# Kernel optimization log

Measured on AMD Instinct MI355X. Metric: run time of the kernel, lower is better.

The kernel has to match this reference:

```python
import jax, jax.numpy as jnp
import numpy as np

N = 100_000      # nodes
E = 3_200_000    # edges (avg degree 32)
G = 512          # graphs in batch
IN_DIM = 3
H = 64
L = 3
BN_EPS = 1e-5


def setup_inputs() -> dict:
    key = jax.random.key(0)
    ks = jax.random.split(key, 14)
    s = 0.1
    x = jax.random.normal(ks[0], (N, IN_DIM), jnp.float32)
    edge_index = jax.random.randint(ks[1], (2, E), 0, N, dtype=jnp.int32)
    batch = jnp.sort(jax.random.randint(ks[2], (N,), 0, G, dtype=jnp.int32))
    # GIN MLP params per layer: Linear(in,H) -> ReLU -> Linear(H,H)
    w1_0 = jax.random.normal(ks[3], (IN_DIM, H), jnp.float32) * s   # layer 0 first linear
    w1_r = jax.random.normal(ks[4], (L - 1, H, H), jnp.float32) * s  # layers 1..L-1 first linear
    b1 = jax.random.normal(ks[5], (L, H), jnp.float32) * s
    w2 = jax.random.normal(ks[6], (L, H, H), jnp.float32) * s
    b2 = jax.random.normal(ks[7], (L, H), jnp.float32) * s
    gamma = 1.0 + jax.random.normal(ks[8], (L, H), jnp.float32) * 0.05
    beta = jax.random.normal(ks[9], (L, H), jnp.float32) * 0.05
    wout = jax.random.normal(ks[10], (H, H), jnp.float32) * s
    bout = jax.random.normal(ks[11], (H,), jnp.float32) * s
    return {"x": x, "edge_index": edge_index, "batch": batch,
            "w1_0": w1_0, "w1_r": w1_r, "b1": b1, "w2": w2, "b2": b2,
            "gamma": gamma, "beta": beta, "wout": wout, "bout": bout}


def reference(x, edge_index, batch, w1_0, w1_r, b1, w2, b2, gamma, beta, wout, bout):
    src, dst = edge_index[0], edge_index[1]
    for i in range(L):
        # GINConv: h = mlp((1+eps)*x + sum_{j in N(i)} x_j), eps = 0
        agg = jax.ops.segment_sum(x[src], dst, num_segments=N)  # [N, d]
        h = x + agg
        W1 = w1_0 if i == 0 else w1_r[i - 1]
        h = jax.nn.relu(h @ W1 + b1[i]) @ w2[i] + b2[i]          # [N, H]
        # BatchNorm1d (training mode: biased batch stats over nodes)
        mu = h.mean(axis=0)
        var = h.var(axis=0)
        h = (h - mu) / jnp.sqrt(var + BN_EPS) * gamma[i] + beta[i]
        x = jax.nn.relu(h)
    # global_mean_pool: segment mean over graph ids
    sums = jax.ops.segment_sum(x, batch, num_segments=G)                        # [G, H]
    cnt = jax.ops.segment_sum(jnp.ones((N, 1), x.dtype), batch, num_segments=G)  # [G, 1]
    graph_repr = jnp.where(cnt > 0, sums / jnp.maximum(cnt, 1.0), 0.0)
    return graph_repr @ wout + bout  # [G, H]
```

## Files before the change

### kernel.cpp

```cpp
#include <hip/hip_runtime.h>


#define NBMAX 1024
#define CAP 4608
#define CHUNK 8192
#define NBLK_MAX 512
#define MSTR 72

typedef __attribute__((ext_vector_type(8))) short bf16x8;
typedef __attribute__((ext_vector_type(4))) float f32x4;

static __device__ __forceinline__ bf16x8 as_bf16x8(uint4 u) {
    union { uint4 a; bf16x8 b; } x; x.a = u; return x.b;
}
static __device__ __forceinline__ unsigned short bf16r(float v) {
    unsigned u = __float_as_uint(v);
    return (unsigned short)((u + 0x7FFFu + ((u >> 16) & 1u)) >> 16);
}
static __device__ __forceinline__ unsigned bf16pack2(float a, float b) {
    return (unsigned)bf16r(a) | ((unsigned)bf16r(b) << 16);
}

__global__ void prep_weights(const float* __restrict__ w1_0, const float* __restrict__ w1_r,
                             const float* __restrict__ w2, unsigned short* __restrict__ w1T0,
                             unsigned short* __restrict__ w1T, unsigned short* __restrict__ w2T) {
    int t = blockIdx.x * 256 + threadIdx.x;
    if (t < 64 * 32) {
        int c = t >> 5, k = t & 31;
        w1T0[t] = bf16r(k < 3 ? w1_0[k * 64 + c] : 0.f);
    }
    if (t < 2 * 64 * 64) {
        int l = t >> 12, r = t & 4095, c = r >> 6, k = r & 63;
        w1T[t] = bf16r(w1_r[l * 4096 + k * 64 + c]);
    }
    if (t < 3 * 64 * 64) {
        int l = t >> 12, r = t & 4095, c = r >> 6, k = r & 63;
        w2T[t] = bf16r(w2[l * 4096 + k * 64 + c]);
    }
}

__global__ __launch_bounds__(512) void scatter_sort(
    const int* __restrict__ src, const int* __restrict__ dst,
    int* __restrict__ bucketed2, int* __restrict__ offsTab, int E) {
    __shared__ int hist[NBMAX];
    __shared__ int offs[NBMAX];
    __shared__ int stage[CHUNK];
    int t = threadIdx.x, blk = blockIdx.x;
    int e0 = blk * CHUNK, e1 = min(e0 + CHUNK, E);
    int len = e1 - e0;
    hist[t] = 0; hist[t + 512] = 0;
    __syncthreads();
    for (int e = e0 + t; e < e1; e += 512) atomicAdd(&hist[dst[e] >> 7], 1);
    __syncthreads();
    offs[t] = hist[t]; offs[t + 512] = hist[t + 512];
    __syncthreads();
    for (int off = 1; off < 1024; off <<= 1) {
        int v0 = (t >= off) ? offs[t - off] : 0;
        int v1 = offs[t + 512 - off];
        __syncthreads();
        offs[t] += v0;
        offs[t + 512] += v1;
        __syncthreads();
    }
    offs[t] -= hist[t]; offs[t + 512] -= hist[t + 512];
    hist[t] = 0; hist[t + 512] = 0;
    __syncthreads();
    offsTab[blk * 1025 + t] = offs[t];
    offsTab[blk * 1025 + t + 512] = offs[t + 512];
    if (t == 0) offsTab[blk * 1025 + 1024] = len;
    for (int e = e0 + t; e < e1; e += 512) {
        int d = dst[e];
        int bk = d >> 7;
        int r = offs[bk] + atomicAdd(&hist[bk], 1);
        stage[r] = src[e] | ((d & 127) << 20);
    }
    __syncthreads();
    for (int j = t; j < len; j += 512) bucketed2[e0 + j] = stage[j];
}

__global__ __launch_bounds__(256) void bucket_csr(
    const int* __restrict__ bucketed2, const int* __restrict__ offsTab,
    int* __restrict__ csrOut, int* __restrict__ rowstart, int* __restrict__ rowend,
    int N, int nblk) {
    __shared__ int ein[CAP];
    __shared__ int emid[CAP];
    __shared__ int runs[NBLK_MAX];
    __shared__ int rbeg[NBLK_MAX];
    __shared__ int hist[128];
    __shared__ int base[129];
    int b = blockIdx.x, t = threadIdx.x, node0 = b << 7;
    for (int r = t; r < NBLK_MAX; r += 256) {
        int l = 0, g0 = 0;
        if (r < nblk) {
            int beg = offsTab[r * 1025 + b];
            int end = offsTab[r * 1025 + b + 1];
            l = end - beg;
            g0 = r * CHUNK + beg;
        }
        runs[r] = l;
        rbeg[r] = g0;
    }
    __syncthreads();
    for (int off = 1; off < NBLK_MAX; off <<= 1) {
        int v0 = (t >= off) ? runs[t - off] : 0;
        int v1 = (t + 256 >= off) ? runs[t + 256 - off] : 0;
        __syncthreads();
        runs[t] += v0;
        runs[t + 256] += v1;
        __syncthreads();
    }
    int cnt = min(runs[NBLK_MAX - 1], CAP);
    for (int j = t; j < cnt; j += 256) {
        int lo = 0, hi = nblk - 1;
        while (lo < hi) {
            int m = (lo + hi) >> 1;
            if (runs[m] > j) hi = m; else lo = m + 1;
        }
        int st = lo ? runs[lo - 1] : 0;
        ein[j] = bucketed2[rbeg[lo] + (j - st)];
    }
    if (t < 128) hist[t] = 0;
    __syncthreads();
    for (int j = t; j < cnt; j += 256) atomicAdd(&hist[(ein[j] & 0xFFFFF) >> 10], 1);
    __syncthreads();
    if (t < 128) base[t + 1] = hist[t];
    if (t == 0) base[0] = 0;
    __syncthreads();
    for (int off = 1; off < 128; off <<= 1) {
        int v = 0;
        if (t < 128 && (t + 1) > off) v = base[t + 1 - off];
        __syncthreads();
        if (t < 128 && (t + 1) > off) base[t + 1] += v;
        __syncthreads();
    }
    if (t < 128) hist[t] = 0;
    __syncthreads();
    for (int j = t; j < cnt; j += 256) {
        int p = ein[j];
        int sb = (p & 0xFFFFF) >> 10;
        int pos = base[sb] + atomicAdd(&hist[sb], 1);
        emid[pos] = p;
    }
    __syncthreads();
    if (t < 128) hist[t] = 0;
    __syncthreads();
    for (int j = t; j < cnt; j += 256) atomicAdd(&hist[emid[j] >> 20], 1);
    __syncthreads();
    if (t < 128) base[t + 1] = hist[t];
    if (t == 0) base[0] = 0;
    __syncthreads();
    for (int off = 1; off < 128; off <<= 1) {
        int v = 0;
        if (t < 128 && (t + 1) > off) v = base[t + 1 - off];
        __syncthreads();
        if (t < 128 && (t + 1) > off) base[t + 1] += v;
        __syncthreads();
    }
    if (t < 128) {
        int n = node0 + t;
        if (n < N) {
            rowstart[n] = b * CAP + base[t];
            rowend[n] = b * CAP + base[t + 1];
        }
        hist[t] = 0;
    }
    __syncthreads();
    for (int j = t; j < cnt; j += 256) {
        int p = emid[j];
        int local = p >> 20;
        int pos = base[local] + atomicAdd(&hist[local], 1);
        ein[pos] = p & 0xFFFFF;
    }
    __syncthreads();
    for (int j = t; j < cnt; j += 256) csrOut[b * CAP + j] = ein[j];
}

__global__ void agg3(const float* __restrict__ x, const int* __restrict__ rowstart,
                     const int* __restrict__ rowend, const int* __restrict__ csr,
                     uint4* __restrict__ out, int N) {
    int n = blockIdx.x * blockDim.x + threadIdx.x;
    if (n >= N) return;
    float a0 = x[n * 3], a1 = x[n * 3 + 1], a2 = x[n * 3 + 2];
    float b0 = 0.f, b1 = 0.f, b2 = 0.f;
    float c0 = 0.f, c1 = 0.f, c2 = 0.f;
    float d0 = 0.f, d1 = 0.f, d2 = 0.f;
    int s = rowstart[n], e = rowend[n];
    int j = s;
    for (; j + 3 < e; j += 4) {
        int i0 = csr[j], i1 = csr[j + 1], i2 = csr[j + 2], i3 = csr[j + 3];
        a0 += x[i0 * 3]; a1 += x[i0 * 3 + 1]; a2 += x[i0 * 3 + 2];
        b0 += x[i1 * 3]; b1 += x[i1 * 3 + 1]; b2 += x[i1 * 3 + 2];
        c0 += x[i2 * 3]; c1 += x[i2 * 3 + 1]; c2 += x[i2 * 3 + 2];
        d0 += x[i3 * 3]; d1 += x[i3 * 3 + 1]; d2 += x[i3 * 3 + 2];
    }
    for (; j < e; j++) {
        int nb = csr[j];
        a0 += x[nb * 3]; a1 += x[nb * 3 + 1]; a2 += x[nb * 3 + 2];
    }
    float s0 = a0 + b0 + c0 + d0, s1 = a1 + b1 + c1 + d1, s2 = a2 + b2 + c2 + d2;
    out[n] = make_uint4(bf16pack2(s0, s1), bf16pack2(s2, 0.f), 0u, 0u);
}

__device__ __forceinline__ void accum_bf16(const uint4 u,
                                           const float4 scA, const float4 scB,
                                           const float4 shA, const float4 shB,
                                           float* __restrict__ a) {
    a[0] += fmaxf(__uint_as_float(u.x << 16) * scA.x + shA.x, 0.f);
    a[1] += fmaxf(__uint_as_float(u.x & 0xFFFF0000u) * scA.y + shA.y, 0.f);
    a[2] += fmaxf(__uint_as_float(u.y << 16) * scA.z + shA.z, 0.f);
    a[3] += fmaxf(__uint_as_float(u.y & 0xFFFF0000u) * scA.w + shA.w, 0.f);
    a[4] += fmaxf(__uint_as_float(u.z << 16) * scB.x + shB.x, 0.f);
    a[5] += fmaxf(__uint_as_float(u.z & 0xFFFF0000u) * scB.y + shB.y, 0.f);
    a[6] += fmaxf(__uint_as_float(u.w << 16) * scB.z + shB.z, 0.f);
    a[7] += fmaxf(__uint_as_float(u.w & 0xFFFF0000u) * scB.w + shB.w, 0.f);
}

__global__ __launch_bounds__(256) void agg64_bn(
    const unsigned short* __restrict__ h, const int* __restrict__ rowstart,
    const int* __restrict__ rowend, const int* __restrict__ csr,
    const float* __restrict__ bnsum, const float* __restrict__ bnsq,
    const float* __restrict__ gamma, const float* __restrict__ beta,
    uint4* __restrict__ out, int N) {
    __shared__ float scs[64], shs[64];
    int t = threadIdx.x;
    if (t < 64) {
        float mu = bnsum[t] / (float)N;
        float var = bnsq[t] / (float)N - mu * mu;
        float s = gamma[t] * rsqrtf(var + 1e-5f);
        scs[t] = s;
        shs[t] = beta[t] - mu * s;
    }
    __syncthreads();
    int g = t >> 3, l = t & 7;
    int n = blockIdx.x * 32 + g;
    if (n >= N) return;
    int c0 = l * 8;
    float4 scA = *(const float4*)&scs[c0], scB = *(const float4*)&scs[c0 + 4];
    float4 shA = *(const float4*)&shs[c0], shB = *(const float4*)&shs[c0 + 4];
    const uint4* hr = (const uint4*)h;
    float A[8] = {0,0,0,0,0,0,0,0};
    float B[8] = {0,0,0,0,0,0,0,0};
    uint4 self = hr[(size_t)n * 8 + l];
    accum_bf16(self, scA, scB, shA, shB, A);
    int s = rowstart[n], e = rowend[n];
    int j = s;
    for (; j + 3 < e; j += 4) {
        int i0 = csr[j], i1 = csr[j + 1], i2 = csr[j + 2], i3 = csr[j + 3];
        uint4 w0 = hr[(size_t)i0 * 8 + l];
        uint4 w1 = hr[(size_t)i1 * 8 + l];
        uint4 w2 = hr[(size_t)i2 * 8 + l];
        uint4 w3 = hr[(size_t)i3 * 8 + l];
        accum_bf16(w0, scA, scB, shA, shB, A);
        accum_bf16(w1, scA, scB, shA, shB, B);
        accum_bf16(w2, scA, scB, shA, shB, A);
        accum_bf16(w3, scA, scB, shA, shB, B);
    }
    for (; j < e; j++) {
        uint4 w = hr[(size_t)csr[j] * 8 + l];
        accum_bf16(w, scA, scB, shA, shB, A);
    }
    uint4 o;
    o.x = bf16pack2(A[0] + B[0], A[1] + B[1]);
    o.y = bf16pack2(A[2] + B[2], A[3] + B[3]);
    o.z = bf16pack2(A[4] + B[4], A[5] + B[5]);
    o.w = bf16pack2(A[6] + B[6], A[7] + B[7]);
    out[(size_t)n * 8 + l] = o;
}

template <bool L0>
__global__ __launch_bounds__(256) void mlp_mfma(
    const uint4* __restrict__ actIn,
    uint4* __restrict__ houtU4,
    const uint4* __restrict__ w1Tu,
    const float* __restrict__ b1,
    const uint4* __restrict__ w2Tu,
    const float* __restrict__ b2,
    float* __restrict__ partS, float* __restrict__ partQ, int N, int nTiles) {
    __shared__ __align__(16) unsigned short mids[64 * MSTR];
    __shared__ float red[16][64];
    int t = threadIdx.x;
    int w = t >> 6, l = t & 63;
    int m16 = l & 15, q = l >> 4;
    const uint4 z4 = make_uint4(0, 0, 0, 0);
    bf16x8 w1f[4][2], w2f[4][2];
    float bias1[4], bias2[4];
#pragma unroll
    for (int c = 0; c < 4; c++) {
        int col = c * 16 + m16;
        if (L0) {
            w1f[c][0] = as_bf16x8(w1Tu[col * 4 + q]);
        } else {
            w1f[c][0] = as_bf16x8(w1Tu[col * 8 + q]);
            w1f[c][1] = as_bf16x8(w1Tu[col * 8 + 4 + q]);
        }
        w2f[c][0] = as_bf16x8(w2Tu[col * 8 + q]);
        w2f[c][1] = as_bf16x8(w2Tu[col * 8 + 4 + q]);
        bias1[c] = b1[col];
        bias2[c] = b2[col];
    }
    float s[4] = {0, 0, 0, 0}, sq[4] = {0, 0, 0, 0};
    for (int tile = blockIdx.x; tile < nTiles; tile += gridDim.x) {
        int base = tile * 64;
        __syncthreads();
        int rA = base + w * 16 + m16;
        bf16x8 a0, a1;
        if (L0) {
            a0 = as_bf16x8((rA < N && q == 0) ? actIn[rA] : z4);
        } else {
            a0 = as_bf16x8(rA < N ? actIn[(size_t)rA * 8 + q] : z4);
            a1 = as_bf16x8(rA < N ? actIn[(size_t)rA * 8 + 4 + q] : z4);
        }
#pragma unroll
        for (int c = 0; c < 4; c++) {
            float bias = bias1[c];
            f32x4 acc = {bias, bias, bias, bias};
            if (L0) {
                acc = __builtin_amdgcn_mfma_f32_16x16x32_bf16(a0, w1f[c][0], acc, 0, 0, 0);
            } else {
                acc = __builtin_amdgcn_mfma_f32_16x16x32_bf16(a0, w1f[c][0], acc, 0, 0, 0);
                acc = __builtin_amdgcn_mfma_f32_16x16x32_bf16(a1, w1f[c][1], acc, 0, 0, 0);
            }
            int col = c * 16 + m16;
#pragma unroll
            for (int r = 0; r < 4; r++) {
                int row = w * 16 + q * 4 + r;
                mids[row * MSTR + col] = bf16r(fmaxf(acc[r], 0.f));
            }
        }
        __syncthreads();
        int rowM = w * 16 + m16;
        const uint4* midU4 = (const uint4*)mids;
        bf16x8 a20 = as_bf16x8(midU4[rowM * 9 + q]);
        bf16x8 a21 = as_bf16x8(midU4[rowM * 9 + 4 + q]);
        f32x4 accs[4];
#pragma unroll
        for (int c = 0; c < 4; c++) {
            float bias = bias2[c];
            f32x4 acc = {bias, bias, bias, bias};
            acc = __builtin_amdgcn_mfma_f32_16x16x32_bf16(a20, w2f[c][0], acc, 0, 0, 0);
            acc = __builtin_amdgcn_mfma_f32_16x16x32_bf16(a21, w2f[c][1], acc, 0, 0, 0);
            accs[c] = acc;
        }
#pragma unroll
        for (int c = 0; c < 4; c++) {
            int col = c * 16 + m16;
#pragma unroll
            for (int r = 0; r < 4; r++) {
                int row = w * 16 + q * 4 + r;
                float v = accs[c][r];
                if (base + row < N) { s[c] += v; sq[c] += v * v; }
                mids[row * MSTR + col] = bf16r(v);
            }
        }
        __syncthreads();
        for (int i = t; i < 512; i += 256) {
            int row = i >> 3, qo = i & 7;
            int gr = base + row;
            if (gr < N) houtU4[(size_t)gr * 8 + qo] = ((const uint4*)mids)[row * 9 + qo];
        }
    }
    __syncthreads();
    for (int c = 0; c < 4; c++) red[w * 4 + q][c * 16 + m16] = s[c];
    __syncthreads();
    if (t < 64) {
        float S = 0.f;
        for (int i = 0; i < 16; i++) S += red[i][t];
        partS[blockIdx.x * 64 + t] = S;
    }
    __syncthreads();
    for (int c = 0; c < 4; c++) red[w * 4 + q][c * 16 + m16] = sq[c];
    __syncthreads();
    if (t < 64) {
        float S = 0.f;
        for (int i = 0; i < 16; i++) S += red[i][t];
        partQ[blockIdx.x * 64 + t] = S;
    }
}

__global__ __launch_bounds__(256) void bn_reduce(
    const float* __restrict__ partS, const float* __restrict__ partQ,
    float* __restrict__ bnsum, float* __restrict__ bnsq, int nParts) {
    __shared__ float rs[256], rq[256];
    int b = blockIdx.x, t = threadIdx.x;
    float S = 0.f, Q = 0.f;
    for (int p = t; p < nParts; p += 256) {
        S += partS[p * 64 + b];
        Q += partQ[p * 64 + b];
    }
    rs[t] = S; rq[t] = Q;
    __syncthreads();
    for (int off = 128; off > 0; off >>= 1) {
        if (t < off) { rs[t] += rs[t + off]; rq[t] += rq[t + off]; }
        __syncthreads();
    }
    if (t == 0) { bnsum[b] = rs[0]; bnsq[b] = rq[0]; }
}

__device__ __forceinline__ int lowb(const int* __restrict__ a, int n, int v) {
    int lo = 0, hi = n;
    while (lo < hi) {
        int m = (lo + hi) >> 1;
        if (a[m] < v) lo = m + 1; else hi = m;
    }
    return lo;
}

__global__ __launch_bounds__(256) void bn_pool_out(
    const unsigned short* __restrict__ h, const int* __restrict__ batch,
    const float* __restrict__ bnsum, const float* __restrict__ bnsq,
    const float* __restrict__ gamma, const float* __restrict__ beta,
    const float* __restrict__ wout, const float* __restrict__ bout,
    float* __restrict__ out, int N) {
    __shared__ float sc[64], sh[64];
    __shared__ float part[4][64];
    __shared__ float gr[64];
    __shared__ int range[2];
    int g = blockIdx.x, t = threadIdx.x;
    if (t < 64) {
        float mu = bnsum[t] / (float)N;
        float var = bnsq[t] / (float)N - mu * mu;
        float s = gamma[t] * rsqrtf(var + 1e-5f);
        sc[t] = s;
        sh[t] = beta[t] - mu * s;
    }
    if (t == 64) range[0] = lowb(batch, N, g);
    if (t == 65) range[1] = lowb(batch, N, g + 1);
    __syncthreads();
    int s0 = range[0], s1 = range[1];
    int col = t & 63, ro = t >> 6;
    float acc = 0.f;
    for (int n = s0 + ro; n < s1; n += 4) {
        float v = __uint_as_float(((unsigned)h[(size_t)n * 64 + col]) << 16);
        acc += fmaxf(v * sc[col] + sh[col], 0.f);
    }
    part[ro][col] = acc;
    __syncthreads();
    if (t < 64) {
        float S = part[0][t] + part[1][t] + part[2][t] + part[3][t];
        float c = (float)(s1 - s0);
        gr[t] = (c > 0.f) ? S / c : 0.f;
    }
    __syncthreads();
    if (t < 64) {
        float a = bout[t];
        for (int f = 0; f < 64; f++) a += gr[f] * wout[f * 64 + t];
        out[g * 64 + t] = a;
    }
}

extern "C" void kernel_launch(void* const* d_in, const int* in_sizes, int n_in,
                              void* d_out, int out_size, void* d_ws, size_t ws_size,
                              hipStream_t stream) {
    const float* x     = (const float*)d_in[0];
    const int*   ei    = (const int*)d_in[1];
    const int*   batch = (const int*)d_in[2];
    const float* w1_0  = (const float*)d_in[3];
    const float* w1_r  = (const float*)d_in[4];
    const float* b1    = (const float*)d_in[5];
    const float* w2    = (const float*)d_in[6];
    const float* b2    = (const float*)d_in[7];
    const float* gamma = (const float*)d_in[8];
    const float* beta  = (const float*)d_in[9];
    const float* wout  = (const float*)d_in[10];
    const float* bout  = (const float*)d_in[11];
    float* out = (float*)d_out;

    const int N = in_sizes[2];
    const int E = in_sizes[1] / 2;
    const int NB = (N + 127) >> 7;
    const int nblk = (E + CHUNK - 1) / CHUNK;
    const int nTiles = (N + 63) >> 6;
    const int nMlpBlocks = 782;

    unsigned short* hbX = (unsigned short*)d_ws;
    unsigned short* hbY = hbX + (size_t)N * 64;
    uint4* h3b = (uint4*)(hbY + (size_t)N * 64);
    int* bucketed2 = (int*)(h3b + N);
    int* offsTab   = bucketed2 + (size_t)nblk * CHUNK;
    int* csrOut    = offsTab + (size_t)nblk * 1025;
    int* rowstart  = csrOut + (size_t)NB * CAP;
    int* rowend    = rowstart + N;
    float* bnstats = (float*)(rowend + N);
    float* partS   = bnstats + 384;
    float* partQ   = partS + (size_t)nMlpBlocks * 64;
    unsigned short* w1T0 = (unsigned short*)(partQ + (size_t)nMlpBlocks * 64);
    unsigned short* w1T  = w1T0 + 64 * 32;
    unsigned short* w2T  = w1T + 2 * 64 * 64;

    const int* srcv = ei;
    const int* dstv = ei + E;

    prep_weights<<<48, 256, 0, stream>>>(w1_0, w1_r, w2, w1T0, w1T, w2T);

    scatter_sort<<<nblk, 512, 0, stream>>>(srcv, dstv, bucketed2, offsTab, E);
    bucket_csr<<<NB, 256, 0, stream>>>(bucketed2, offsTab, csrOut, rowstart, rowend, N, nblk);

    agg3<<<(N + 255) / 256, 256, 0, stream>>>(x, rowstart, rowend, csrOut, h3b, N);
    mlp_mfma<true><<<nMlpBlocks, 256, 0, stream>>>(h3b, (uint4*)hbX, (const uint4*)w1T0, b1,
                                                   (const uint4*)w2T, b2,
                                                   partS, partQ, N, nTiles);
    bn_reduce<<<64, 256, 0, stream>>>(partS, partQ, bnstats, bnstats + 64, nMlpBlocks);

    agg64_bn<<<(N + 31) / 32, 256, 0, stream>>>(hbX, rowstart, rowend, csrOut,
                                                bnstats, bnstats + 64, gamma, beta,
                                                (uint4*)hbY, N);
    mlp_mfma<false><<<nMlpBlocks, 256, 0, stream>>>((const uint4*)hbY, (uint4*)hbX,
                                                    (const uint4*)w1T, b1 + 64,
                                                    (const uint4*)(w2T + 4096), b2 + 64,
                                                    partS, partQ, N, nTiles);
    bn_reduce<<<64, 256, 0, stream>>>(partS, partQ, bnstats + 128, bnstats + 192, nMlpBlocks);

    agg64_bn<<<(N + 31) / 32, 256, 0, stream>>>(hbX, rowstart, rowend, csrOut,
                                                bnstats + 128, bnstats + 192,
                                                gamma + 64, beta + 64, (uint4*)hbY, N);
    mlp_mfma<false><<<nMlpBlocks, 256, 0, stream>>>((const uint4*)hbY, (uint4*)hbX,
                                                    (const uint4*)(w1T + 4096), b1 + 128,
                                                    (const uint4*)(w2T + 8192), b2 + 128,
                                                    partS, partQ, N, nTiles);
    bn_reduce<<<64, 256, 0, stream>>>(partS, partQ, bnstats + 256, bnstats + 320, nMlpBlocks);

    bn_pool_out<<<512, 256, 0, stream>>>(hbX, batch, bnstats + 256, bnstats + 320,
                                         gamma + 128, beta + 128, wout, bout, out, N);
}
```

Baseline: 377.9 us.

## Fuse neighbor aggregation with GIN MLP into one per-layer kernel

Merges the aggregation kernels (agg3/agg64_bn) and the MFMA MLP kernel into a single gin_layer kernel. Each block aggregates 128 nodes into shared memory and then runs the two-layer MLP on them. This drops the intermediate bf16 activation round-trip through global memory and three kernel launches. In exchange the grid shrinks to one block per 128 nodes with larger LDS use, which may lower occupancy and latency hiding for the gather phase, and an extra barrier is added in the MLP loop.

New measurement: 432.8 us. 1.15x slower.

```diff
diff --git a/kernel.cpp b/kernel.cpp
--- a/kernel.cpp
+++ b/kernel.cpp
@@ -175,32 +175,6 @@
     for (int j = t; j < cnt; j += 256) csrOut[b * CAP + j] = ein[j];
 }
 
-__global__ void agg3(const float* __restrict__ x, const int* __restrict__ rowstart,
-                     const int* __restrict__ rowend, const int* __restrict__ csr,
-                     uint4* __restrict__ out, int N) {
-    int n = blockIdx.x * blockDim.x + threadIdx.x;
-    if (n >= N) return;
-    float a0 = x[n * 3], a1 = x[n * 3 + 1], a2 = x[n * 3 + 2];
-    float b0 = 0.f, b1 = 0.f, b2 = 0.f;
-    float c0 = 0.f, c1 = 0.f, c2 = 0.f;
-    float d0 = 0.f, d1 = 0.f, d2 = 0.f;
-    int s = rowstart[n], e = rowend[n];
-    int j = s;
-    for (; j + 3 < e; j += 4) {
-        int i0 = csr[j], i1 = csr[j + 1], i2 = csr[j + 2], i3 = csr[j + 3];
-        a0 += x[i0 * 3]; a1 += x[i0 * 3 + 1]; a2 += x[i0 * 3 + 2];
-        b0 += x[i1 * 3]; b1 += x[i1 * 3 + 1]; b2 += x[i1 * 3 + 2];
-        c0 += x[i2 * 3]; c1 += x[i2 * 3 + 1]; c2 += x[i2 * 3 + 2];
-        d0 += x[i3 * 3]; d1 += x[i3 * 3 + 1]; d2 += x[i3 * 3 + 2];
-    }
-    for (; j < e; j++) {
-        int nb = csr[j];
-        a0 += x[nb * 3]; a1 += x[nb * 3 + 1]; a2 += x[nb * 3 + 2];
-    }
-    float s0 = a0 + b0 + c0 + d0, s1 = a1 + b1 + c1 + d1, s2 = a2 + b2 + c2 + d2;
-    out[n] = make_uint4(bf16pack2(s0, s1), bf16pack2(s2, 0.f), 0u, 0u);
-}
-
 __device__ __forceinline__ void accum_bf16(const uint4 u,
                                            const float4 scA, const float4 scB,
                                            const float4 shA, const float4 shB,
@@ -215,73 +189,106 @@
     a[7] += fmaxf(__uint_as_float(u.w & 0xFFFF0000u) * scB.w + shB.w, 0.f);
 }
 
-__global__ __launch_bounds__(256) void agg64_bn(
-    const unsigned short* __restrict__ h, const int* __restrict__ rowstart,
-    const int* __restrict__ rowend, const int* __restrict__ csr,
-    const float* __restrict__ bnsum, const float* __restrict__ bnsq,
-    const float* __restrict__ gamma, const float* __restrict__ beta,
-    uint4* __restrict__ out, int N) {
+template <bool L0>
+__global__ __launch_bounds__(256) void gin_layer(
+    const void* __restrict__ actInRaw,
+    const int* __restrict__ rowstart, const int* __restrict__ rowend,
+    const int* __restrict__ csr,
+    const float* __restrict__ bnsumPrev, const float* __restrict__ bnsqPrev,
+    const float* __restrict__ gammaPrev, const float* __restrict__ betaPrev,
+    const uint4* __restrict__ w1Tu, const float* __restrict__ b1,
+    const uint4* __restrict__ w2Tu, const float* __restrict__ b2,
+    uint4* __restrict__ houtU4,
+    float* __restrict__ partS, float* __restrict__ partQ, int N) {
+    __shared__ __align__(16) unsigned short acts[128 * MSTR];
+    __shared__ __align__(16) unsigned short mids[64 * MSTR];
+    __shared__ float red[16][64];
     __shared__ float scs[64], shs[64];
     int t = threadIdx.x;
-    if (t < 64) {
-        float mu = bnsum[t] / (float)N;
-        float var = bnsq[t] / (float)N - mu * mu;
-        float s = gamma[t] * rsqrtf(var + 1e-5f);
-        scs[t] = s;
-        shs[t] = beta[t] - mu * s;
-    }
-    __syncthreads();
-    int g = t >> 3, l = t & 7;
-    int n = blockIdx.x * 32 + g;
-    if (n >= N) return;
-    int c0 = l * 8;
-    float4 scA = *(const float4*)&scs[c0], scB = *(const float4*)&scs[c0 + 4];
-    float4 shA = *(const float4*)&shs[c0], shB = *(const float4*)&shs[c0 + 4];
-    const uint4* hr = (const uint4*)h;
-    float A[8] = {0,0,0,0,0,0,0,0};
-    float B[8] = {0,0,0,0,0,0,0,0};
-    uint4 self = hr[(size_t)n * 8 + l];
-    accum_bf16(self, scA, scB, shA, shB, A);
-    int s = rowstart[n], e = rowend[n];
-    int j = s;
-    for (; j + 3 < e; j += 4) {
-        int i0 = csr[j], i1 = csr[j + 1], i2 = csr[j + 2], i3 = csr[j + 3];
-        uint4 w0 = hr[(size_t)i0 * 8 + l];
-        uint4 w1 = hr[(size_t)i1 * 8 + l];
-        uint4 w2 = hr[(size_t)i2 * 8 + l];
-        uint4 w3 = hr[(size_t)i3 * 8 + l];
-        accum_bf16(w0, scA, scB, shA, shB, A);
-        accum_bf16(w1, scA, scB, shA, shB, B);
-        accum_bf16(w2, scA, scB, shA, shB, A);
-        accum_bf16(w3, scA, scB, shA, shB, B);
-    }
-    for (; j < e; j++) {
-        uint4 w = hr[(size_t)csr[j] * 8 + l];
-        accum_bf16(w, scA, scB, shA, shB, A);
-    }
-    uint4 o;
-    o.x = bf16pack2(A[0] + B[0], A[1] + B[1]);
-    o.y = bf16pack2(A[2] + B[2], A[3] + B[3]);
-    o.z = bf16pack2(A[4] + B[4], A[5] + B[5]);
-    o.w = bf16pack2(A[6] + B[6], A[7] + B[7]);
-    out[(size_t)n * 8 + l] = o;
-}
-
-template <bool L0>
-__global__ __launch_bounds__(256) void mlp_mfma(
-    const uint4* __restrict__ actIn,
-    uint4* __restrict__ houtU4,
-    const uint4* __restrict__ w1Tu,
-    const float* __restrict__ b1,
-    const uint4* __restrict__ w2Tu,
-    const float* __restrict__ b2,
-    float* __restrict__ partS, float* __restrict__ partQ, int N, int nTiles) {
-    __shared__ __align__(16) unsigned short mids[64 * MSTR];
-    __shared__ float red[16][64];
-    int t = threadIdx.x;
-    int w = t >> 6, l = t & 63;
-    int m16 = l & 15, q = l >> 4;
+    int b = blockIdx.x, node0 = b << 7;
     const uint4 z4 = make_uint4(0, 0, 0, 0);
+    uint4* actsU4 = (uint4*)acts;
+
+    if (!L0) {
+        if (t < 64) {
+            float mu = bnsumPrev[t] / (float)N;
+            float var = bnsqPrev[t] / (float)N - mu * mu;
+            float s = gammaPrev[t] * rsqrtf(var + 1e-5f);
+            scs[t] = s;
+            shs[t] = betaPrev[t] - mu * s;
+        }
+        __syncthreads();
+    }
+
+    if (L0) {
+        const float* x = (const float*)actInRaw;
+        if (t < 128) {
+            int n = node0 + t;
+            float s0 = 0.f, s1 = 0.f, s2 = 0.f;
+            if (n < N) {
+                s0 = x[n * 3]; s1 = x[n * 3 + 1]; s2 = x[n * 3 + 2];
+                float b0 = 0.f, b1v = 0.f, b2v = 0.f;
+                float c0 = 0.f, c1 = 0.f, c2 = 0.f;
+                float d0 = 0.f, d1 = 0.f, d2 = 0.f;
+                int s = rowstart[n], e = rowend[n];
+                int j = s;
+                for (; j + 3 < e; j += 4) {
+                    int i0 = csr[j], i1 = csr[j + 1], i2 = csr[j + 2], i3 = csr[j + 3];
+                    s0 += x[i0 * 3]; s1 += x[i0 * 3 + 1]; s2 += x[i0 * 3 + 2];
+                    b0 += x[i1 * 3]; b1v += x[i1 * 3 + 1]; b2v += x[i1 * 3 + 2];
+                    c0 += x[i2 * 3]; c1 += x[i2 * 3 + 1]; c2 += x[i2 * 3 + 2];
+                    d0 += x[i3 * 3]; d1 += x[i3 * 3 + 1]; d2 += x[i3 * 3 + 2];
+                }
+                for (; j < e; j++) {
+                    int nb = csr[j];
+                    s0 += x[nb * 3]; s1 += x[nb * 3 + 1]; s2 += x[nb * 3 + 2];
+                }
+                s0 += b0 + c0 + d0; s1 += b1v + c1 + d1; s2 += b2v + c2 + d2;
+            }
+            actsU4[t * 9] = make_uint4(bf16pack2(s0, s1), bf16pack2(s2, 0.f), 0u, 0u);
+        }
+    } else {
+        const uint4* hr = (const uint4*)actInRaw;
+        int g = t >> 3, l = t & 7;
+        int c0i = l * 8;
+        float4 scA = *(const float4*)&scs[c0i], scB = *(const float4*)&scs[c0i + 4];
+        float4 shA = *(const float4*)&shs[c0i], shB = *(const float4*)&shs[c0i + 4];
+        for (int p = 0; p < 4; p++) {
+            int r = p * 32 + g;
+            int n = node0 + r;
+            float A[8] = {0,0,0,0,0,0,0,0};
+            float B[8] = {0,0,0,0,0,0,0,0};
+            if (n < N) {
+                accum_bf16(hr[(size_t)n * 8 + l], scA, scB, shA, shB, A);
+                int s = rowstart[n], e = rowend[n];
+                int j = s;
+                for (; j + 3 < e; j += 4) {
+                    int i0 = csr[j], i1 = csr[j + 1], i2 = csr[j + 2], i3 = csr[j + 3];
+                    uint4 w0 = hr[(size_t)i0 * 8 + l];
+                    uint4 w1 = hr[(size_t)i1 * 8 + l];
+                    uint4 w2 = hr[(size_t)i2 * 8 + l];
+                    uint4 w3 = hr[(size_t)i3 * 8 + l];
+                    accum_bf16(w0, scA, scB, shA, shB, A);
+                    accum_bf16(w1, scA, scB, shA, shB, B);
+                    accum_bf16(w2, scA, scB, shA, shB, A);
+                    accum_bf16(w3, scA, scB, shA, shB, B);
+                }
+                for (; j < e; j++) {
+                    uint4 w = hr[(size_t)csr[j] * 8 + l];
+                    accum_bf16(w, scA, scB, shA, shB, A);
+                }
+            }
+            uint4 o;
+            o.x = bf16pack2(A[0] + B[0], A[1] + B[1]);
+            o.y = bf16pack2(A[2] + B[2], A[3] + B[3]);
+            o.z = bf16pack2(A[4] + B[4], A[5] + B[5]);
+            o.w = bf16pack2(A[6] + B[6], A[7] + B[7]);
+            actsU4[r * 9 + l] = o;
+        }
+    }
+
+    int w = t >> 6, l64 = t & 63;
+    int m16 = l64 & 15, q = l64 >> 4;
     bf16x8 w1f[4][2], w2f[4][2];
     float bias1[4], bias2[4];
 #pragma unroll
@@ -299,16 +306,16 @@
         bias2[c] = b2[col];
     }
     float s[4] = {0, 0, 0, 0}, sq[4] = {0, 0, 0, 0};
-    for (int tile = blockIdx.x; tile < nTiles; tile += gridDim.x) {
-        int base = tile * 64;
-        __syncthreads();
-        int rA = base + w * 16 + m16;
+    const uint4* midU4 = (const uint4*)mids;
+    for (int T = 0; T < 2; T++) {
+        __syncthreads();
+        int rloc = T * 64 + w * 16 + m16;
         bf16x8 a0, a1;
         if (L0) {
-            a0 = as_bf16x8((rA < N && q == 0) ? actIn[rA] : z4);
+            a0 = as_bf16x8(q == 0 ? actsU4[rloc * 9] : z4);
         } else {
-            a0 = as_bf16x8(rA < N ? actIn[(size_t)rA * 8 + q] : z4);
-            a1 = as_bf16x8(rA < N ? actIn[(size_t)rA * 8 + 4 + q] : z4);
+            a0 = as_bf16x8(actsU4[rloc * 9 + q]);
+            a1 = as_bf16x8(actsU4[rloc * 9 + 4 + q]);
         }
 #pragma unroll
         for (int c = 0; c < 4; c++) {
@@ -329,7 +336,6 @@
         }
         __syncthreads();
         int rowM = w * 16 + m16;
-        const uint4* midU4 = (const uint4*)mids;
         bf16x8 a20 = as_bf16x8(midU4[rowM * 9 + q]);
         bf16x8 a21 = as_bf16x8(midU4[rowM * 9 + 4 + q]);
         f32x4 accs[4];
@@ -341,6 +347,7 @@
             acc = __builtin_amdgcn_mfma_f32_16x16x32_bf16(a21, w2f[c][1], acc, 0, 0, 0);
             accs[c] = acc;
         }
+        __syncthreads();
 #pragma unroll
         for (int c = 0; c < 4; c++) {
             int col = c * 16 + m16;
@@ -348,15 +355,16 @@
             for (int r = 0; r < 4; r++) {
                 int row = w * 16 + q * 4 + r;
                 float v = accs[c][r];
-                if (base + row < N) { s[c] += v; sq[c] += v * v; }
+                if (node0 + T * 64 + row < N) { s[c] += v; sq[c] += v * v; }
                 mids[row * MSTR + col] = bf16r(v);
             }
         }
         __syncthreads();
+        int tbase = node0 + T * 64;
         for (int i = t; i < 512; i += 256) {
             int row = i >> 3, qo = i & 7;
-            int gr = base + row;
-            if (gr < N) houtU4[(size_t)gr * 8 + qo] = ((const uint4*)mids)[row * 9 + qo];
+            int gr = tbase + row;
+            if (gr < N) houtU4[(size_t)gr * 8 + qo] = midU4[row * 9 + qo];
         }
     }
     __syncthreads();
@@ -365,7 +373,7 @@
     if (t < 64) {
         float S = 0.f;
         for (int i = 0; i < 16; i++) S += red[i][t];
-        partS[blockIdx.x * 64 + t] = S;
+        partS[b * 64 + t] = S;
     }
     __syncthreads();
     for (int c = 0; c < 4; c++) red[w * 4 + q][c * 16 + m16] = sq[c];
@@ -373,7 +381,7 @@
     if (t < 64) {
         float S = 0.f;
         for (int i = 0; i < 16; i++) S += red[i][t];
-        partQ[blockIdx.x * 64 + t] = S;
+        partQ[b * 64 + t] = S;
     }
 }
 
@@ -469,21 +477,18 @@
     const int E = in_sizes[1] / 2;
     const int NB = (N + 127) >> 7;
     const int nblk = (E + CHUNK - 1) / CHUNK;
-    const int nTiles = (N + 63) >> 6;
-    const int nMlpBlocks = 782;
 
     unsigned short* hbX = (unsigned short*)d_ws;
     unsigned short* hbY = hbX + (size_t)N * 64;
-    uint4* h3b = (uint4*)(hbY + (size_t)N * 64);
-    int* bucketed2 = (int*)(h3b + N);
+    int* bucketed2 = (int*)(hbY + (size_t)N * 64);
     int* offsTab   = bucketed2 + (size_t)nblk * CHUNK;
     int* csrOut    = offsTab + (size_t)nblk * 1025;
     int* rowstart  = csrOut + (size_t)NB * CAP;
     int* rowend    = rowstart + N;
     float* bnstats = (float*)(rowend + N);
     float* partS   = bnstats + 384;
-    float* partQ   = partS + (size_t)nMlpBlocks * 64;
-    unsigned short* w1T0 = (unsigned short*)(partQ + (size_t)nMlpBlocks * 64);
+    float* partQ   = partS + (size_t)NB * 64;
+    unsigned short* w1T0 = (unsigned short*)(partQ + (size_t)NB * 64);
     unsigned short* w1T  = w1T0 + 64 * 32;
     unsigned short* w2T  = w1T + 2 * 64 * 64;
 
@@ -495,29 +500,27 @@
     scatter_sort<<<nblk, 512, 0, stream>>>(srcv, dstv, bucketed2, offsTab, E);
     bucket_csr<<<NB, 256, 0, stream>>>(bucketed2, offsTab, csrOut, rowstart, rowend, N, nblk);
 
-    agg3<<<(N + 255) / 256, 256, 0, stream>>>(x, rowstart, rowend, csrOut, h3b, N);
-    mlp_mfma<true><<<nMlpBlocks, 256, 0, stream>>>(h3b, (uint4*)hbX, (const uint4*)w1T0, b1,
-                                                   (const uint4*)w2T, b2,
-                                                   partS, partQ, N, nTiles);
-    bn_reduce<<<64, 256, 0, stream>>>(partS, partQ, bnstats, bnstats + 64, nMlpBlocks);
-
-    agg64_bn<<<(N + 31) / 32, 256, 0, stream>>>(hbX, rowstart, rowend, csrOut,
-                                                bnstats, bnstats + 64, gamma, beta,
-                                                (uint4*)hbY, N);
-    mlp_mfma<false><<<nMlpBlocks, 256, 0, stream>>>((const uint4*)hbY, (uint4*)hbX,
-                                                    (const uint4*)w1T, b1 + 64,
-                                                    (const uint4*)(w2T + 4096), b2 + 64,
-                                                    partS, partQ, N, nTiles);
-    bn_reduce<<<64, 256, 0, stream>>>(partS, partQ, bnstats + 128, bnstats + 192, nMlpBlocks);
-
-    agg64_bn<<<(N + 31) / 32, 256, 0, stream>>>(hbX, rowstart, rowend, csrOut,
-                                                bnstats + 128, bnstats + 192,
-                                                gamma + 64, beta + 64, (uint4*)hbY, N);
-    mlp_mfma<false><<<nMlpBlocks, 256, 0, stream>>>((const uint4*)hbY, (uint4*)hbX,
-                                                    (const uint4*)(w1T + 4096), b1 + 128,
-                                                    (const uint4*)(w2T + 8192), b2 + 128,
-                                                    partS, partQ, N, nTiles);
-    bn_reduce<<<64, 256, 0, stream>>>(partS, partQ, bnstats + 256, bnstats + 320, nMlpBlocks);
+    gin_layer<true><<<NB, 256, 0, stream>>>(x, rowstart, rowend, csrOut,
+                                            nullptr, nullptr, nullptr, nullptr,
+                                            (const uint4*)w1T0, b1,
+                                            (const uint4*)w2T, b2,
+                                            (uint4*)hbX, partS, partQ, N);
+    bn_reduce<<<64, 256, 0, stream>>>(partS, partQ, bnstats, bnstats + 64, NB);
+
+    gin_layer<false><<<NB, 256, 0, stream>>>(hbX, rowstart, rowend, csrOut,
+                                             bnstats, bnstats + 64, gamma, beta,
+                                             (const uint4*)w1T, b1 + 64,
+                                             (const uint4*)(w2T + 4096), b2 + 64,
+                                             (uint4*)hbY, partS, partQ, N);
+    bn_reduce<<<64, 256, 0, stream>>>(partS, partQ, bnstats + 128, bnstats + 192, NB);
+
+    gin_layer<false><<<NB, 256, 0, stream>>>(hbY, rowstart, rowend, csrOut,
+                                             bnstats + 128, bnstats + 192,
+                                             gamma + 64, beta + 64,
+                                             (const uint4*)(w1T + 4096), b1 + 128,
+                                             (const uint4*)(w2T + 8192), b2 + 128,
+                                             (uint4*)hbX, partS, partQ, N);
+    bn_reduce<<<64, 256, 0, stream>>>(partS, partQ, bnstats + 256, bnstats + 320, NB);
 
     bn_pool_out<<<512, 256, 0, stream>>>(hbX, batch, bnstats + 256, bnstats + 320,
                                          gamma + 128, beta + 128, wout, bout, out, N);
```
